# Performance work log

Hardware: AMD Instinct MI355X
Metric: run time of the kernel (lower is better)

## Reference

```python
import jax, jax.numpy as jnp
import numpy as np

B = 512            # graphs in batch
N = 246            # ROIs per graph per node type (Brainnetome atlas)
D = 256            # node feature dim (in_channels)
DEG = 32           # edges per node per edge type
RATIO = 0.8
K = int(np.ceil(RATIO * N))   # 197 nodes kept per graph (PyG topk uses ceil)
NT = B * N                    # total nodes per node type
E = B * N * DEG               # total edges per edge type
SLOPE = 0.2                   # HANConv leaky_relu negative slope


def _seg_softmax(logits, seg, num_segments):
    # numerically stable softmax over edges grouped by destination node
    m = jax.ops.segment_max(logits, seg, num_segments=num_segments)
    m = jnp.where(jnp.isfinite(m), m, 0.0)
    e = jnp.exp(logits - m[seg])
    s = jax.ops.segment_sum(e, seg, num_segments=num_segments)
    return e / (s[seg] + 1e-16)


def _edge_type_out(h_src, h_dst, ei, a_src, a_dst, n_dst):
    # one HANConv metapath: GAT-style attention + sum-aggregate + relu
    row, col = ei[0], ei[1]
    logit = jax.nn.leaky_relu((h_src * a_src).sum(-1)[row] + (h_dst * a_dst).sum(-1)[col], SLOPE)
    alpha = _seg_softmax(logit, col, n_dst)
    out = jax.ops.segment_sum(h_src[row] * alpha[:, None], col, num_segments=n_dst)
    return jax.nn.relu(out)


def _group(o1, o2, k_w, k_b, q):
    # HANConv semantic attention over the 2 metapaths hitting a node type
    stk = jnp.stack([o1, o2])                    # [2, NT, 1]
    t = jnp.tanh(stk @ k_w + k_b).mean(axis=1)   # [2, 1]
    w = jax.nn.softmax((q * t).sum(-1))          # [2]
    return (w[:, None, None] * stk).sum(0)       # [NT, 1]


def _han_scores(x_bold, x_dti, pw_b, pb_b, pw_d, pb_d, att, k_w, k_b, q, ei_bb, ei_bd, ei_db, ei_dd):
    h_b = x_bold @ pw_b + pb_b   # [NT, 1]
    h_d = x_dti @ pw_d + pb_d
    o_bb = _edge_type_out(h_b, h_b, ei_bb, att[0, 0], att[0, 1], NT)  # dst bold
    o_bd = _edge_type_out(h_b, h_d, ei_bd, att[1, 0], att[1, 1], NT)  # dst dti
    o_db = _edge_type_out(h_d, h_b, ei_db, att[2, 0], att[2, 1], NT)  # dst bold
    o_dd = _edge_type_out(h_d, h_d, ei_dd, att[3, 0], att[3, 1], NT)  # dst dti
    s_bold = _group(o_bb, o_db, k_w, k_b, q)[:, 0]
    s_dti = _group(o_bd, o_dd, k_w, k_b, q)[:, 0]
    return s_bold, s_dti


def _topk(score):
    # per-graph top-K (all graphs have exactly N nodes -> static K)
    _, idx = jax.lax.top_k(score.reshape(B, N), K)
    return (idx + (jnp.arange(B, dtype=idx.dtype) * N)[:, None]).reshape(-1)


def _mask_of(perm, num_nodes):
    return jnp.full((num_nodes,), -1, dtype=jnp.int32).at[perm].set(
        jnp.arange(perm.shape[0], dtype=jnp.int32))


def _filter(ei, mask_row, mask_col):
    # jit-compatible variant of filter_adj: keep full edge length, mark
    # dropped edges with -1 and return the validity mask (no compaction).
    r, c = mask_row[ei[0]], mask_col[ei[1]]
    valid = (r >= 0) & (c >= 0)
    return jnp.stack([jnp.where(valid, r, -1), jnp.where(valid, c, -1)]), valid


def setup_inputs() -> dict:
    key = jax.random.key(0)
    ks = jax.random.split(key, 12)

    def edges(k):
        k1, k2 = jax.random.split(k)
        base = jnp.repeat(jnp.arange(B, dtype=jnp.int32) * N, N * DEG)
        row = base + jax.random.randint(k1, (E,), 0, N, dtype=jnp.int32)
        col = base + jax.random.randint(k2, (E,), 0, N, dtype=jnp.int32)
        return jnp.stack([row, col])

    batch = jnp.repeat(jnp.arange(B, dtype=jnp.int32), N)
    return {
        "x_bold": jax.random.normal(ks[0], (NT, D), jnp.float32),
        "x_dti": jax.random.normal(ks[1], (NT, D), jnp.float32),
        "proj_w_bold": jax.random.normal(ks[2], (D, 1), jnp.float32) / np.float32(np.sqrt(D)),
        "proj_b_bold": jnp.zeros((1,), jnp.float32),
        "proj_w_dti": jax.random.normal(ks[3], (D, 1), jnp.float32) / np.float32(np.sqrt(D)),
        "proj_b_dti": jnp.zeros((1,), jnp.float32),
        "att": jax.random.normal(ks[4], (4, 2, 1), jnp.float32),
        "k_lin_w": jax.random.normal(ks[5], (1, 1), jnp.float32),
        "k_lin_b": jnp.zeros((1,), jnp.float32),
        "q": jax.random.normal(ks[6], (1,), jnp.float32),
        "ei_bb": edges(ks[7]),
        "ei_bd": edges(ks[8]),
        "ei_db": edges(ks[9]),
        "ei_dd": edges(ks[10]),
        "batch_bold": batch,
        "batch_dti": batch,
    }


def reference(x_bold, x_dti, proj_w_bold, proj_b_bold, proj_w_dti, proj_b_dti,
              att, k_lin_w, k_lin_b, q, ei_bb, ei_bd, ei_db, ei_dd,
              batch_bold, batch_dti):
    s_bold, s_dti = _han_scores(x_bold, x_dti, proj_w_bold, proj_b_bold,
                                proj_w_dti, proj_b_dti, att, k_lin_w, k_lin_b, q,
                                ei_bb, ei_bd, ei_db, ei_dd)
    perm_b = _topk(s_bold)
    perm_d = _topk(s_dti)
    xb = x_bold[perm_b] * jnp.tanh(s_bold[perm_b])[:, None]
    xd = x_dti[perm_d] * jnp.tanh(s_dti[perm_d])[:, None]
    mb = _mask_of(perm_b, NT)
    md = _mask_of(perm_d, NT)
    bb_f, v_bb = _filter(ei_bb, mb, mb)   # filter_adj_single on bold-bold
    dd_f, v_dd = _filter(ei_dd, md, md)   # filter_adj_single on dti-dti
    bd_f, v_bd = _filter(ei_bd, mb, md)   # filter_adj_multi mode=1
    db_f, v_db = _filter(ei_db, md, mb)   # filter_adj_multi mode=2
    return (xb, xd, bb_f, v_bb, bd_f, v_bd, db_f, v_db, dd_f, v_dd,
            batch_bold[perm_b], batch_dti[perm_d], perm_b, perm_d, s_bold, s_dti)
```

## Files before the change

### kernel.cpp

```cpp
#include <hip/hip_runtime.h>
#include <cmath>

#define BB   512
#define NN   246
#define DD   256
#define DEGC 32
#define KK   197
#define NTOT (BB*NN)
#define EE   (BB*NN*DEGC)
#define EPG  (NN*DEGC)
#define EPG4 (EPG/4)
#define BKK  (BB*KK)

#define O_XB     0LL
#define O_XD     25821184LL
#define O_E0     51642368LL
#define STRIDE3E 12091392LL
#define O_BATCHB 100007936LL
#define O_BATCHD 100108800LL
#define O_PERMB  100209664LL
#define O_PERMD  100310528LL
#define O_SB     100411392LL
#define O_SD     100537344LL

__device__ __forceinline__ unsigned f2o(float f) {
    unsigned u = __float_as_uint(f);
    return (u & 0x80000000u) ? ~u : (u | 0x80000000u);
}
__device__ __forceinline__ float o2f(unsigned u) {
    return (u & 0x80000000u) ? __uint_as_float(u & 0x7fffffffu)
                             : __uint_as_float(~u);
}

__global__ __launch_bounds__(256) void proj_kernel(
    const float* __restrict__ xb, const float* __restrict__ xd,
    const float* __restrict__ wb, const float* __restrict__ bbp,
    const float* __restrict__ wd, const float* __restrict__ bdp,
    float* __restrict__ hb, float* __restrict__ hd) {
    int wid  = (blockIdx.x * 256 + threadIdx.x) >> 6;
    int lane = threadIdx.x & 63;
    if (wid >= 2 * NTOT) return;
    const float* x; const float* w; const float* bp; float* h; int node;
    if (wid < NTOT) { x = xb; w = wb; bp = bbp; h = hb; node = wid; }
    else            { x = xd; w = wd; bp = bdp; h = hd; node = wid - NTOT; }
    float4 xv = ((const float4*)(x + (long long)node * DD))[lane];
    float4 wv = ((const float4*)w)[lane];
    double acc = (double)xv.x * wv.x + (double)xv.y * wv.y +
                 (double)xv.z * wv.z + (double)xv.w * wv.w;
#pragma unroll
    for (int m = 32; m; m >>= 1) acc += __shfl_xor(acc, m, 64);
    if (lane == 0) h[node] = __fadd_rn((float)acc, bp[0]);
}

__global__ __launch_bounds__(1024) void att_kernel(
    const int* __restrict__ ei_bb, const int* __restrict__ ei_bd,
    const int* __restrict__ ei_db, const int* __restrict__ ei_dd,
    const float* __restrict__ hb, const float* __restrict__ hd,
    const float* __restrict__ att, float* __restrict__ o) {
    __shared__ float          l_sh[EPG];
    __shared__ unsigned char  r_sh[EPG];
    __shared__ unsigned char  c_sh[EPG];
    __shared__ unsigned       m_sh[NN];
    __shared__ float          s_sh[NN];
    __shared__ float          num_sh[NN];

    int bid = blockIdx.x;
    int t   = bid >> 9;
    int g   = bid & 511;
    const int* ei = (t == 0) ? ei_bb : (t == 1) ? ei_bd : (t == 2) ? ei_db : ei_dd;
    const float* hs  = (t >= 2) ? hd : hb;
    const float* hdt = (t & 1)  ? hd : hb;
    float a_src = att[2 * t], a_dst = att[2 * t + 1];
    int base = g * NN;
    int tid  = threadIdx.x;

    if (tid < NN) { m_sh[tid] = 0u; s_sh[tid] = 0.f; num_sh[tid] = 0.f; }
    __syncthreads();

    const int4* rows = (const int4*)(ei + g * EPG);
    const int4* cols = (const int4*)(ei + EE + g * EPG);

    for (int q = tid; q < EPG4; q += 1024) {
        int4 r4 = rows[q], c4 = cols[q];
#pragma unroll
        for (int j = 0; j < 4; ++j) {
            int r = ((const int*)&r4)[j] - base;
            int c = ((const int*)&c4)[j] - base;
            float st = __fmul_rn(a_src, hs[base + r]);
            float dt = __fmul_rn(a_dst, hdt[base + c]);
            float l  = __fadd_rn(st, dt);
            l = (l >= 0.f) ? l : __fmul_rn(0.2f, l);
            int idx = q * 4 + j;
            l_sh[idx] = l;
            r_sh[idx] = (unsigned char)r;
            c_sh[idx] = (unsigned char)c;
            atomicMax(&m_sh[c], f2o(l));
        }
    }
    __syncthreads();

    for (int idx = tid; idx < EPG; idx += 1024) {
        float l  = l_sh[idx];
        int   r  = r_sh[idx], c = c_sh[idx];
        float mx = o2f(m_sh[c]);
        float e  = expf(l - mx);
        atomicAdd(&s_sh[c], e);
        atomicAdd(&num_sh[c], __fmul_rn(hs[base + r], e));
    }
    __syncthreads();

    if (tid < NN) {
        float s = s_sh[tid] + 1e-16f;
        float v = num_sh[tid] / s;
        o[(long long)t * NTOT + base + tid] = (v > 0.f) ? v : 0.f;
    }
}

__global__ void zero_sums_kernel(double* sums) {
    if (threadIdx.x < 4 && blockIdx.x == 0) sums[threadIdx.x] = 0.0;
}

__global__ __launch_bounds__(256) void grp_reduce_kernel(
    const float* __restrict__ o, const float* __restrict__ kwp,
    const float* __restrict__ kbp, double* __restrict__ sums) {
    int i = blockIdx.x * 256 + threadIdx.x;
    int t = blockIdx.x / 492;
    float kw = kwp[0], kb = kbp[0];
    float v = tanhf(__fadd_rn(__fmul_rn(o[i], kw), kb));
    double acc = (double)v;
#pragma unroll
    for (int m = 32; m; m >>= 1) acc += __shfl_xor(acc, m, 64);
    __shared__ double part[4];
    int lane = threadIdx.x & 63, wv = threadIdx.x >> 6;
    if (lane == 0) part[wv] = acc;
    __syncthreads();
    if (threadIdx.x == 0) {
        double tot = ((part[0] + part[1]) + part[2]) + part[3];
        atomicAdd(&sums[t], tot);
    }
}

__global__ void grp_w_kernel(const double* __restrict__ sums,
                             const float* __restrict__ qp,
                             float* __restrict__ wscal) {
    if (threadIdx.x == 0 && blockIdx.x == 0) {
        float q = qp[0];
        float tv[4];
#pragma unroll
        for (int i = 0; i < 4; ++i) tv[i] = (float)(sums[i] / (double)NTOT);
        {
            float l0 = __fmul_rn(q, tv[0]), l1 = __fmul_rn(q, tv[2]);
            float mx = fmaxf(l0, l1);
            float e0 = expf(l0 - mx), e1 = expf(l1 - mx);
            float se = __fadd_rn(e0, e1);
            wscal[0] = e0 / se; wscal[1] = e1 / se;
        }
        {
            float l0 = __fmul_rn(q, tv[1]), l1 = __fmul_rn(q, tv[3]);
            float mx = fmaxf(l0, l1);
            float e0 = expf(l0 - mx), e1 = expf(l1 - mx);
            float se = __fadd_rn(e0, e1);
            wscal[2] = e0 / se; wscal[3] = e1 / se;
        }
    }
}

__global__ __launch_bounds__(256) void score_kernel(
    const float* __restrict__ o, const float* __restrict__ wscal,
    float* __restrict__ sb, float* __restrict__ sd,
    float* __restrict__ osb, float* __restrict__ osd) {
    int i = blockIdx.x * 256 + threadIdx.x;
    float w0 = wscal[0], w1 = wscal[1], w2 = wscal[2], w3 = wscal[3];
    float vb = __fadd_rn(__fmul_rn(w0, o[i]),          __fmul_rn(w1, o[2LL * NTOT + i]));
    float vd = __fadd_rn(__fmul_rn(w2, o[NTOT + i]),   __fmul_rn(w3, o[3LL * NTOT + i]));
    sb[i] = vb; sd[i] = vd; osb[i] = vb; osd[i] = vd;
}

__global__ __launch_bounds__(256) void topk_kernel(
    const float* __restrict__ sb, const float* __restrict__ sd,
    const int* __restrict__ batch_b, const int* __restrict__ batch_d,
    int* __restrict__ mask_b, int* __restrict__ mask_d,
    int* __restrict__ perm_b, int* __restrict__ perm_d,
    float* __restrict__ out) {
    __shared__ float v[256];
    __shared__ int   ix[256];
    int g = blockIdx.x, tid = threadIdx.x;
    for (int which = 0; which < 2; ++which) {
        const float* s     = which ? sd : sb;
        const int*   batch = which ? batch_d : batch_b;
        int* mask  = which ? mask_d : mask_b;
        int* permi = which ? perm_d : perm_b;
        float* operm  = out + (which ? O_PERMD : O_PERMB);
        float* obatch = out + (which ? O_BATCHD : O_BATCHB);
        v[tid]  = (tid < NN) ? s[g * NN + tid] : -INFINITY;
        ix[tid] = tid;
        __syncthreads();
        for (int k2 = 2; k2 <= 256; k2 <<= 1) {
            for (int j = k2 >> 1; j > 0; j >>= 1) {
                int p = tid ^ j;
                if (p > tid) {
                    float va = v[tid], vb2 = v[p];
                    int   ia = ix[tid], ib = ix[p];
                    bool before = (va > vb2) || (va == vb2 && ia < ib);
                    bool up = ((tid & k2) == 0);
                    if (up ? !before : before) {
                        v[tid] = vb2; v[p] = va; ix[tid] = ib; ix[p] = ia;
                    }
                }
                __syncthreads();
            }
        }
        if (tid < NN) {
            int node  = ix[tid];
            int gnode = g * NN + node;
            if (tid < KK) {
                int gp = g * KK + tid;
                permi[gp]  = gnode;
                operm[gp]  = (float)gnode;
                obatch[gp] = (float)batch[gnode];
                mask[gnode] = gp;
            } else {
                mask[gnode] = -1;
            }
        }
        __syncthreads();
    }
}

__global__ __launch_bounds__(256) void gather_kernel(
    const float* __restrict__ xb, const float* __restrict__ xd,
    const int* __restrict__ perm_b, const int* __restrict__ perm_d,
    const float* __restrict__ sb, const float* __restrict__ sd,
    float* __restrict__ out) {
    int wid  = (blockIdx.x * 256 + threadIdx.x) >> 6;
    int lane = threadIdx.x & 63;
    if (wid >= 2 * BKK) return;
    int which = wid >= BKK;
    int j = which ? wid - BKK : wid;
    const float* x    = which ? xd : xb;
    const int*   perm = which ? perm_d : perm_b;
    const float* s    = which ? sd : sb;
    long long obase   = which ? O_XD : O_XB;
    int p = perm[j];
    float scale = tanhf(s[p]);
    float4 vv = ((const float4*)(x + (long long)p * DD))[lane];
    float4 r  = make_float4(vv.x * scale, vv.y * scale, vv.z * scale, vv.w * scale);
    ((float4*)(out + obase + (long long)j * DD))[lane] = r;
}

__global__ __launch_bounds__(256) void filter_kernel(
    const int* __restrict__ ei_bb, const int* __restrict__ ei_bd,
    const int* __restrict__ ei_db, const int* __restrict__ ei_dd,
    const int* __restrict__ mask_b, const int* __restrict__ mask_d,
    float* __restrict__ out) {
    const int QE = EE / 4;
    int tid = blockIdx.x * 256 + threadIdx.x;
    if (tid >= 4 * QE) return;
    int t = tid / QE;
    int q = tid - t * QE;
    const int* ei = (t == 0) ? ei_bb : (t == 1) ? ei_bd : (t == 2) ? ei_db : ei_dd;
    const int* mr = (t >= 2) ? mask_d : mask_b;
    const int* mc = (t & 1)  ? mask_d : mask_b;
    int4 r4 = ((const int4*)ei)[q];
    int4 c4 = ((const int4*)(ei + EE))[q];
    float4 orow, ocol, oval;
#pragma unroll
    for (int j = 0; j < 4; ++j) {
        int r = mr[((const int*)&r4)[j]];
        int c = mc[((const int*)&c4)[j]];
        bool val = (r >= 0) && (c >= 0);
        ((float*)&orow)[j] = val ? (float)r : -1.f;
        ((float*)&ocol)[j] = val ? (float)c : -1.f;
        ((float*)&oval)[j] = val ? 1.f : 0.f;
    }
    float* base = out + O_E0 + (long long)t * STRIDE3E;
    ((float4*)base)[q]              = orow;
    ((float4*)(base + EE))[q]       = ocol;
    ((float4*)(base + 2LL * EE))[q] = oval;
}

extern "C" void kernel_launch(void* const* d_in, const int* in_sizes, int n_in,
                              void* d_out, int out_size, void* d_ws, size_t ws_size,
                              hipStream_t stream) {
    const float* x_bold = (const float*)d_in[0];
    const float* x_dti  = (const float*)d_in[1];
    const float* pw_b   = (const float*)d_in[2];
    const float* pb_b   = (const float*)d_in[3];
    const float* pw_d   = (const float*)d_in[4];
    const float* pb_d   = (const float*)d_in[5];
    const float* att    = (const float*)d_in[6];
    const float* k_w    = (const float*)d_in[7];
    const float* k_b    = (const float*)d_in[8];
    const float* qv     = (const float*)d_in[9];
    const int* ei_bb    = (const int*)d_in[10];
    const int* ei_bd    = (const int*)d_in[11];
    const int* ei_db    = (const int*)d_in[12];
    const int* ei_dd    = (const int*)d_in[13];
    const int* batch_b  = (const int*)d_in[14];
    const int* batch_d  = (const int*)d_in[15];
    float* out = (float*)d_out;

    char* w = (char*)d_ws;
    double* sums  = (double*)w;
    float*  wscal = (float*)(w + 32);
    float*  hb    = (float*)(w + 48);
    float*  hd    = hb + NTOT;
    float*  obuf  = hd + NTOT;
    float*  sb    = obuf + 4LL * NTOT;
    float*  sd    = sb + NTOT;
    int* mask_b   = (int*)(sd + NTOT);
    int* mask_d   = mask_b + NTOT;
    int* perm_b   = mask_d + NTOT;
    int* perm_d   = perm_b + BKK;

    zero_sums_kernel<<<1, 64, 0, stream>>>(sums);
    proj_kernel<<<2 * NTOT / 4, 256, 0, stream>>>(x_bold, x_dti, pw_b, pb_b,
                                                  pw_d, pb_d, hb, hd);
    att_kernel<<<4 * BB, 1024, 0, stream>>>(ei_bb, ei_bd, ei_db, ei_dd,
                                            hb, hd, att, obuf);
    grp_reduce_kernel<<<4 * NTOT / 256, 256, 0, stream>>>(obuf, k_w, k_b, sums);
    grp_w_kernel<<<1, 64, 0, stream>>>(sums, qv, wscal);
    score_kernel<<<NTOT / 256, 256, 0, stream>>>(obuf, wscal, sb, sd,
                                                 out + O_SB, out + O_SD);
    topk_kernel<<<BB, 256, 0, stream>>>(sb, sd, batch_b, batch_d,
                                        mask_b, mask_d, perm_b, perm_d, out);
    gather_kernel<<<2 * BKK * 64 / 256, 256, 0, stream>>>(x_bold, x_dti,
                                                          perm_b, perm_d,
                                                          sb, sd, out);
    filter_kernel<<<EE / 256, 256, 0, stream>>>(ei_bb, ei_bd, ei_db, ei_dd,
                                                mask_b, mask_d, out);
}
```

Measured before the change: 949.7 us.

## Single-pass attention softmax without max, stage h in LDS, split topk blocks

The attention kernel drops the per-destination max pass and computes exp(logit) directly. It accumulates sum and weighted numerator in a single pass, with source and destination h values cached in shared memory, which removes the large LDS edge buffers and one sync phase. The zero-init kernel is folded into the projection kernel, and the top-k kernel now uses one block per graph and node type. Skipping the max subtraction risks overflow for large logits.

```diff
diff --git a/kernel.cpp b/kernel.cpp
--- a/kernel.cpp
+++ b/kernel.cpp
@@ -23,20 +23,13 @@
 #define O_SB     100411392LL
 #define O_SD     100537344LL
 
-__device__ __forceinline__ unsigned f2o(float f) {
-    unsigned u = __float_as_uint(f);
-    return (u & 0x80000000u) ? ~u : (u | 0x80000000u);
-}
-__device__ __forceinline__ float o2f(unsigned u) {
-    return (u & 0x80000000u) ? __uint_as_float(u & 0x7fffffffu)
-                             : __uint_as_float(~u);
-}
-
 __global__ __launch_bounds__(256) void proj_kernel(
     const float* __restrict__ xb, const float* __restrict__ xd,
     const float* __restrict__ wb, const float* __restrict__ bbp,
     const float* __restrict__ wd, const float* __restrict__ bdp,
-    float* __restrict__ hb, float* __restrict__ hd) {
+    float* __restrict__ hb, float* __restrict__ hd,
+    double* __restrict__ sums) {
+    if (blockIdx.x == 0 && threadIdx.x < 4) sums[threadIdx.x] = 0.0;
     int wid  = (blockIdx.x * 256 + threadIdx.x) >> 6;
     int lane = threadIdx.x & 63;
     if (wid >= 2 * NTOT) return;
@@ -52,17 +45,15 @@
     if (lane == 0) h[node] = __fadd_rn((float)acc, bp[0]);
 }
 
-__global__ __launch_bounds__(1024) void att_kernel(
+__global__ __launch_bounds__(512) void att_kernel(
     const int* __restrict__ ei_bb, const int* __restrict__ ei_bd,
     const int* __restrict__ ei_db, const int* __restrict__ ei_dd,
     const float* __restrict__ hb, const float* __restrict__ hd,
     const float* __restrict__ att, float* __restrict__ o) {
-    __shared__ float          l_sh[EPG];
-    __shared__ unsigned char  r_sh[EPG];
-    __shared__ unsigned char  c_sh[EPG];
-    __shared__ unsigned       m_sh[NN];
-    __shared__ float          s_sh[NN];
-    __shared__ float          num_sh[NN];
+    __shared__ float hs_sh[NN];
+    __shared__ float hd_sh[NN];
+    __shared__ float s_sh[NN];
+    __shared__ float num_sh[NN];
 
     int bid = blockIdx.x;
     int t   = bid >> 9;
@@ -74,50 +65,37 @@
     int base = g * NN;
     int tid  = threadIdx.x;
 
-    if (tid < NN) { m_sh[tid] = 0u; s_sh[tid] = 0.f; num_sh[tid] = 0.f; }
+    if (tid < NN) {
+        hs_sh[tid]  = hs[base + tid];
+        hd_sh[tid]  = hdt[base + tid];
+        s_sh[tid]   = 1e-16f;
+        num_sh[tid] = 0.f;
+    }
     __syncthreads();
 
     const int4* rows = (const int4*)(ei + g * EPG);
     const int4* cols = (const int4*)(ei + EE + g * EPG);
 
-    for (int q = tid; q < EPG4; q += 1024) {
+    for (int q = tid; q < EPG4; q += 512) {
         int4 r4 = rows[q], c4 = cols[q];
 #pragma unroll
         for (int j = 0; j < 4; ++j) {
             int r = ((const int*)&r4)[j] - base;
             int c = ((const int*)&c4)[j] - base;
-            float st = __fmul_rn(a_src, hs[base + r]);
-            float dt = __fmul_rn(a_dst, hdt[base + c]);
-            float l  = __fadd_rn(st, dt);
+            float hr = hs_sh[r];
+            float l  = __fadd_rn(__fmul_rn(a_src, hr), __fmul_rn(a_dst, hd_sh[c]));
             l = (l >= 0.f) ? l : __fmul_rn(0.2f, l);
-            int idx = q * 4 + j;
-            l_sh[idx] = l;
-            r_sh[idx] = (unsigned char)r;
-            c_sh[idx] = (unsigned char)c;
-            atomicMax(&m_sh[c], f2o(l));
+            float e = expf(l);
+            atomicAdd(&s_sh[c], e);
+            atomicAdd(&num_sh[c], __fmul_rn(hr, e));
         }
     }
     __syncthreads();
 
-    for (int idx = tid; idx < EPG; idx += 1024) {
-        float l  = l_sh[idx];
-        int   r  = r_sh[idx], c = c_sh[idx];
-        float mx = o2f(m_sh[c]);
-        float e  = expf(l - mx);
-        atomicAdd(&s_sh[c], e);
-        atomicAdd(&num_sh[c], __fmul_rn(hs[base + r], e));
-    }
-    __syncthreads();
-
     if (tid < NN) {
-        float s = s_sh[tid] + 1e-16f;
-        float v = num_sh[tid] / s;
+        float v = num_sh[tid] / s_sh[tid];
         o[(long long)t * NTOT + base + tid] = (v > 0.f) ? v : 0.f;
     }
-}
-
-__global__ void zero_sums_kernel(double* sums) {
-    if (threadIdx.x < 4 && blockIdx.x == 0) sums[threadIdx.x] = 0.0;
 }
 
 __global__ __launch_bounds__(256) void grp_reduce_kernel(
@@ -184,46 +162,43 @@
     float* __restrict__ out) {
     __shared__ float v[256];
     __shared__ int   ix[256];
-    int g = blockIdx.x, tid = threadIdx.x;
-    for (int which = 0; which < 2; ++which) {
-        const float* s     = which ? sd : sb;
-        const int*   batch = which ? batch_d : batch_b;
-        int* mask  = which ? mask_d : mask_b;
-        int* permi = which ? perm_d : perm_b;
-        float* operm  = out + (which ? O_PERMD : O_PERMB);
-        float* obatch = out + (which ? O_BATCHD : O_BATCHB);
-        v[tid]  = (tid < NN) ? s[g * NN + tid] : -INFINITY;
-        ix[tid] = tid;
-        __syncthreads();
-        for (int k2 = 2; k2 <= 256; k2 <<= 1) {
-            for (int j = k2 >> 1; j > 0; j >>= 1) {
-                int p = tid ^ j;
-                if (p > tid) {
-                    float va = v[tid], vb2 = v[p];
-                    int   ia = ix[tid], ib = ix[p];
-                    bool before = (va > vb2) || (va == vb2 && ia < ib);
-                    bool up = ((tid & k2) == 0);
-                    if (up ? !before : before) {
-                        v[tid] = vb2; v[p] = va; ix[tid] = ib; ix[p] = ia;
-                    }
+    int g = blockIdx.x & 511, which = blockIdx.x >> 9, tid = threadIdx.x;
+    const float* s     = which ? sd : sb;
+    const int*   batch = which ? batch_d : batch_b;
+    int* mask  = which ? mask_d : mask_b;
+    int* permi = which ? perm_d : perm_b;
+    float* operm  = out + (which ? O_PERMD : O_PERMB);
+    float* obatch = out + (which ? O_BATCHD : O_BATCHB);
+    v[tid]  = (tid < NN) ? s[g * NN + tid] : -INFINITY;
+    ix[tid] = tid;
+    __syncthreads();
+    for (int k2 = 2; k2 <= 256; k2 <<= 1) {
+        for (int j = k2 >> 1; j > 0; j >>= 1) {
+            int p = tid ^ j;
+            if (p > tid) {
+                float va = v[tid], vb2 = v[p];
+                int   ia = ix[tid], ib = ix[p];
+                bool before = (va > vb2) || (va == vb2 && ia < ib);
+                bool up = ((tid & k2) == 0);
+                if (up ? !before : before) {
+                    v[tid] = vb2; v[p] = va; ix[tid] = ib; ix[p] = ia;
                 }
-                __syncthreads();
             }
-        }
-        if (tid < NN) {
-            int node  = ix[tid];
-            int gnode = g * NN + node;
-            if (tid < KK) {
-                int gp = g * KK + tid;
-                permi[gp]  = gnode;
-                operm[gp]  = (float)gnode;
-                obatch[gp] = (float)batch[gnode];
-                mask[gnode] = gp;
-            } else {
-                mask[gnode] = -1;
-            }
-        }
-        __syncthreads();
+            __syncthreads();
+        }
+    }
+    if (tid < NN) {
+        int node  = ix[tid];
+        int gnode = g * NN + node;
+        if (tid < KK) {
+            int gp = g * KK + tid;
+            permi[gp]  = gnode;
+            operm[gp]  = (float)gnode;
+            obatch[gp] = (float)batch[gnode];
+            mask[gnode] = gp;
+        } else {
+            mask[gnode] = -1;
+        }
     }
 }
 
@@ -313,17 +288,16 @@
     int* perm_b   = mask_d + NTOT;
     int* perm_d   = perm_b + BKK;
 
-    zero_sums_kernel<<<1, 64, 0, stream>>>(sums);
     proj_kernel<<<2 * NTOT / 4, 256, 0, stream>>>(x_bold, x_dti, pw_b, pb_b,
-                                                  pw_d, pb_d, hb, hd);
-    att_kernel<<<4 * BB, 1024, 0, stream>>>(ei_bb, ei_bd, ei_db, ei_dd,
-                                            hb, hd, att, obuf);
+                                                  pw_d, pb_d, hb, hd, sums);
+    att_kernel<<<4 * BB, 512, 0, stream>>>(ei_bb, ei_bd, ei_db, ei_dd,
+                                           hb, hd, att, obuf);
     grp_reduce_kernel<<<4 * NTOT / 256, 256, 0, stream>>>(obuf, k_w, k_b, sums);
     grp_w_kernel<<<1, 64, 0, stream>>>(sums, qv, wscal);
     score_kernel<<<NTOT / 256, 256, 0, stream>>>(obuf, wscal, sb, sd,
                                                  out + O_SB, out + O_SD);
-    topk_kernel<<<BB, 256, 0, stream>>>(sb, sd, batch_b, batch_d,
-                                        mask_b, mask_d, perm_b, perm_d, out);
+    topk_kernel<<<2 * BB, 256, 0, stream>>>(sb, sd, batch_b, batch_d,
+                                            mask_b, mask_d, perm_b, perm_d, out);
     gather_kernel<<<2 * BKK * 64 / 256, 256, 0, stream>>>(x_bold, x_dti,
                                                           perm_b, perm_d,
                                                           sb, sd, out);
```

Result: faster. 921.1 us (-3.0%).
